# Performance work log

Hardware: AMD Instinct MI355X
Metric: run time of the kernel (lower is better)

Reference implementation:

```python
import jax, jax.numpy as jnp
import numpy as np

D_MODEL = 768
D_AU = 5
D_VIS = 20
BOT = 64
WIN = 7
SCALE = 1.0 / np.sqrt(BOT).astype(np.float32)


def layernorm(x, w, b, eps=1e-5):
    mu = jnp.mean(x, axis=-1, keepdims=True)
    var = jnp.mean(jnp.square(x - mu), axis=-1, keepdims=True)
    return (x - mu) * jax.lax.rsqrt(var + eps) * w + b


def proximity_bias_matrix(prox_bias, L_a, L_v):
    # |i * (L_v/L_a) - j|, floored to int; gather into learned table, -inf outside window
    ai = jnp.arange(L_a, dtype=jnp.float32) * (L_v / L_a)  # [L_a]
    vj = jnp.arange(L_v, dtype=jnp.float32)                # [L_v]
    dist = jnp.floor(jnp.abs(ai[:, None] - vj[None, :])).astype(jnp.int32)  # [L_a, L_v]
    within = dist <= WIN
    gathered = prox_bias[jnp.clip(dist, 0, 2 * WIN)]
    return jnp.where(within, gathered, -jnp.inf)


def setup_inputs() -> dict:
    key = jax.random.key(0)
    ks = jax.random.split(key, 32)
    B, L_t, L_v, L_a = 32, 1024, 1024, 2048
    std = 0.02
    inp = {
        'x_text': jax.random.normal(ks[0], (B, L_t, D_MODEL), jnp.float32),
        'video_features': jax.random.normal(ks[1], (B, L_v, D_VIS), jnp.float32),
        'audio_features': jax.random.normal(ks[2], (B, L_a, D_AU), jnp.float32),
        # adapter input LayerNorm (BERT init: weight=1, bias=0)
        'ln_w': jnp.ones((D_MODEL,), jnp.float32),
        'ln_b': jnp.zeros((D_MODEL,), jnp.float32),
        # down projections (torch Linear: [out, in])
        'dpa_w': std * jax.random.normal(ks[3], (BOT, D_AU), jnp.float32),
        'dpa_b': jnp.zeros((BOT,), jnp.float32),
        'dpv_w': std * jax.random.normal(ks[4], (BOT, D_VIS), jnp.float32),
        'dpv_b': jnp.zeros((BOT,), jnp.float32),
        # audio->video cross attention
        'wq_a': std * jax.random.normal(ks[5], (BOT, BOT), jnp.float32),
        'wk_v': std * jax.random.normal(ks[6], (BOT, BOT), jnp.float32),
        'wv_v': std * jax.random.normal(ks[7], (BOT, BOT), jnp.float32),
        'prox_bias': jnp.zeros((2 * WIN + 1,), jnp.float32),
        # fusion MLP + LN
        'fln_w': jnp.ones((2 * BOT,), jnp.float32),
        'fln_b': jnp.zeros((2 * BOT,), jnp.float32),
        'w1f_w': std * jax.random.normal(ks[8], (BOT, 2 * BOT), jnp.float32),
        'w1f_b': jnp.zeros((BOT,), jnp.float32),
        'w2f_w': std * jax.random.normal(ks[9], (BOT, BOT), jnp.float32),
        'w2f_b': jnp.zeros((BOT,), jnp.float32),
        # text->sync alignment attention
        'wq_t': std * jax.random.normal(ks[10], (BOT, D_MODEL), jnp.float32),
        'wk_s': std * jax.random.normal(ks[11], (BOT, BOT), jnp.float32),
        'wv_s': std * jax.random.normal(ks[12], (BOT, BOT), jnp.float32),
        # up projection + learnable scalar
        'up_w': std * jax.random.normal(ks[13], (D_MODEL, BOT), jnp.float32),
        'up_b': jnp.zeros((D_MODEL,), jnp.float32),
        'scale': jnp.ones((1,), jnp.float32),
    }
    return inp


def reference(x_text, video_features, audio_features, ln_w, ln_b, dpa_w, dpa_b,
              dpv_w, dpv_b, wq_a, wk_v, wv_v, prox_bias, fln_w, fln_b,
              w1f_w, w1f_b, w2f_w, w2f_b, wq_t, wk_s, wv_s, up_w, up_b, scale):
    L_v = video_features.shape[1]
    L_a = audio_features.shape[1]
    # adapter_layernorm_option == 'in'
    xt = layernorm(x_text, ln_w, ln_b)
    # down projections + ReLU
    H_v = jax.nn.relu(jnp.einsum('bvf,df->bvd', video_features, dpv_w) + dpv_b)
    H_a = jax.nn.relu(jnp.einsum('baf,df->bad', audio_features, dpa_w) + dpa_b)
    # audio queries attend to video keys/values with proximity bias
    Q_a = jnp.einsum('bad,ed->bae', H_a, wq_a)
    K_v = jnp.einsum('bvd,ed->bve', H_v, wk_v)
    V_v = jnp.einsum('bvd,ed->bve', H_v, wv_v)
    scores = jnp.einsum('bad,bvd->bav', Q_a, K_v) * SCALE
    scores = scores + proximity_bias_matrix(prox_bias, L_a, L_v)[None]
    A = jax.nn.softmax(scores, axis=-1)  # dropout: eval-mode identity
    H_v_tilde = jnp.einsum('bav,bvd->bad', A, V_v)
    # fusion
    H_av = jnp.concatenate([H_a, H_v_tilde], axis=-1)  # [B, L_a, 2*BOT]
    H_av_n = layernorm(H_av, fln_w, fln_b)
    H_fused = jax.nn.relu(jnp.einsum('bac,dc->bad', H_av_n, w1f_w) + w1f_b)
    H_sync = jnp.einsum('bad,ed->bae', H_fused, w2f_w) + w2f_b
    # text -> sync alignment attention
    Q_t = jnp.einsum('btm,dm->btd', xt, wq_t)
    K_s = jnp.einsum('bad,ed->bae', H_sync, wk_s)
    V_s = jnp.einsum('bad,ed->bae', H_sync, wv_s)
    align = jax.nn.softmax(jnp.einsum('btd,bad->bta', Q_t, K_s) * SCALE, axis=-1)
    H_align = jnp.einsum('bta,bad->btd', align, V_s)
    up = jnp.einsum('btd,md->btm', H_align, up_w) + up_b
    return up * scale
```

## Files before the change

kernel.cpp:

```cpp
#include <hip/hip_runtime.h>

typedef unsigned short u16;
typedef unsigned int u32;

using frag8 = __attribute__((ext_vector_type(8))) short;
using facc4 = __attribute__((ext_vector_type(4))) float;

__device__ __forceinline__ float b2f(u16 u) {
  union { u32 i; float f; } v; v.i = ((u32)u) << 16; return v.f;
}
__device__ __forceinline__ u16 f2b(float f) {
  union { float f; u32 i; } v; v.f = f;
  u32 u = v.i;
  return (u16)((u + 0x7FFFu + ((u >> 16) & 1u)) >> 16);
}
__device__ __forceinline__ float ldin(const void* p, size_t i, bool bf) {
  return bf ? b2f(((const u16*)p)[i]) : ((const float*)p)[i];
}
__device__ __forceinline__ u16 ldb(const void* p, size_t i, bool bf) {
  return bf ? ((const u16*)p)[i] : f2b(((const float*)p)[i]);
}
__device__ __forceinline__ bool dt_bf16(const void* ones) {
  return *(const u32*)ones == 0x3F803F80u;
}
__device__ __forceinline__ void gload_lds16(const void* g, void* l) {
  __builtin_amdgcn_global_load_lds(
      (__attribute__((address_space(1))) void*)(g),
      (__attribute__((address_space(3))) void*)(l), 16, 0, 0);
}

#define LT 1024
#define LV 1024
#define LA 2048
#define DM 768

#define W_QA 0
#define W_KV 4096
#define W_VV 8192
#define W_1F 12288
#define W_2F 20480
#define W_KS 24576
#define W_VS 28672
#define W_UP 32768
#define W_QT 81920
#define W_TOT 131072

__global__ __launch_bounds__(256) void k_prep(
    const void* __restrict__ wqa, const void* __restrict__ wkv, const void* __restrict__ wvv,
    const void* __restrict__ w1f, const void* __restrict__ w2f,
    const void* __restrict__ wks, const void* __restrict__ wvs,
    const void* __restrict__ wup, const void* __restrict__ wqt, const void* __restrict__ lnw,
    u16* __restrict__ W)
{
  bool bf = dt_bf16(lnw);
  int idx = blockIdx.x * 256 + threadIdx.x;
  if (idx >= W_TOT) return;
  u16 v;
  if      (idx < W_KV) v = ldb(wqa, idx - W_QA, bf);
  else if (idx < W_VV) v = ldb(wkv, idx - W_KV, bf);
  else if (idx < W_1F) v = ldb(wvv, idx - W_VV, bf);
  else if (idx < W_2F) v = ldb(w1f, idx - W_1F, bf);
  else if (idx < W_KS) v = ldb(w2f, idx - W_2F, bf);
  else if (idx < W_VS) v = ldb(wks, idx - W_KS, bf);
  else if (idx < W_UP) v = ldb(wvs, idx - W_VS, bf);
  else if (idx < W_QT) v = ldb(wup, idx - W_UP, bf);
  else {
    int r = idx - W_QT;
    int k = r - (r / DM) * DM;
    v = f2b(ldin(wqt, r, bf) * ldin(lnw, k, bf));
  }
  W[idx] = v;
}

__global__ __launch_bounds__(256) void k_const(
    const u16* __restrict__ W, const void* __restrict__ wqt, const void* __restrict__ lnb,
    const void* __restrict__ dtp, float* __restrict__ CC)
{
  bool bf = dt_bf16(dtp);
  int j = blockIdx.x * 8 + (threadIdx.x >> 5);
  int lane32 = threadIdx.x & 31;
  float s = 0.f;
  if (j < 64) {
    for (int k = lane32; k < DM; k += 32) s += b2f(W[W_QT + (size_t)j * DM + k]);
  } else {
    int e = j - 64;
    for (int k = lane32; k < DM; k += 32)
      s += ldin(lnb, k, bf) * ldin(wqt, (size_t)e * DM + k, bf);
  }
#pragma unroll
  for (int m = 1; m < 32; m <<= 1) s += __shfl_xor(s, m);
  if (lane32 == 0) CC[j] = s;
}

__global__ __launch_bounds__(256) void k_video(
    const void* __restrict__ vid, const void* __restrict__ dpv_w, const void* __restrict__ dpv_b,
    const u16* __restrict__ W, const void* __restrict__ dtp,
    u16* __restrict__ KvG, u16* __restrict__ VvTG)
{
  bool bf = dt_bf16(dtp);
  __shared__ float vidT[20][72];
  __shared__ float dpvT[20][72];
  __shared__ float dpvB[64];
  __shared__ u16 hvL[64][72];
  __shared__ u16 ksS[64][72];
  __shared__ u16 vsS[64][72];
  int tid = threadIdx.x;
  int b = blockIdx.x >> 4, v0 = (blockIdx.x & 15) << 6;
  for (int c = tid; c < 1280; c += 256) {
    int row = c / 20, d = c - row * 20;
    vidT[d][row] = ldin(vid, (size_t)(b * LV + v0) * 20 + c, bf);
    dpvT[d][row] = ldin(dpv_w, c, bf);
  }
  if (tid < 64) dpvB[tid] = ldin(dpv_b, tid, bf);
  __syncthreads();
  int w = tid >> 6, ln = tid & 63;
  int quad = ln >> 4, l16 = ln & 15;
  for (int rr = 0; rr < 16; ++rr) {
    int row = w * 16 + rr;
    float h = dpvB[ln];
#pragma unroll
    for (int d = 0; d < 20; ++d) h += vidT[d][row] * dpvT[d][ln];
    hvL[row][ln] = f2b(fmaxf(h, 0.f));
  }
  facc4 ka[4] = {}, va[4] = {};
#pragma unroll
  for (int kk = 0; kk < 2; ++kk) {
    frag8 af = *(const frag8*)&hvL[w * 16 + l16][kk * 32 + quad * 8];
#pragma unroll
    for (int nt = 0; nt < 4; ++nt) {
      frag8 bk = *(const frag8*)(W + W_KV + (size_t)(nt * 16 + l16) * 64 + kk * 32 + quad * 8);
      frag8 bv = *(const frag8*)(W + W_VV + (size_t)(nt * 16 + l16) * 64 + kk * 32 + quad * 8);
      ka[nt] = __builtin_amdgcn_mfma_f32_16x16x32_bf16(af, bk, ka[nt], 0, 0, 0);
      va[nt] = __builtin_amdgcn_mfma_f32_16x16x32_bf16(af, bv, va[nt], 0, 0, 0);
    }
  }
#pragma unroll
  for (int nt = 0; nt < 4; ++nt)
#pragma unroll
    for (int r = 0; r < 4; ++r) {
      int row = w * 16 + quad * 4 + r;
      ksS[row][nt * 16 + l16] = f2b(ka[nt][r]);
      vsS[row][nt * 16 + l16] = f2b(va[nt][r]);
    }
  __syncthreads();
  for (int c = tid; c < 2048; c += 256) {
    int row = c >> 5, sg = c & 31;
    u32 v = (u32)ksS[row][sg * 2] | ((u32)ksS[row][sg * 2 + 1] << 16);
    *(u32*)(KvG + (size_t)(b * LV + v0 + row) * 64 + sg * 2) = v;
  }
  for (int c = tid; c < 2048; c += 256) {
    int e = c >> 5, sg = c & 31;
    u32 v = (u32)vsS[sg * 2][e] | ((u32)vsS[sg * 2 + 1][e] << 16);
    *(u32*)(VvTG + (size_t)(b * 64 + e) * LV + v0 + sg * 2) = v;
  }
}

__global__ __launch_bounds__(256, 2) void k_lnqt(
    const void* __restrict__ x, const u16* __restrict__ W, const float* __restrict__ CC,
    const void* __restrict__ dtp, u16* __restrict__ Qt)
{
  bool bf = dt_bf16(dtp);
  int tid = threadIdx.x;
  int w = tid >> 6, ln = tid & 63;
  int quad = ln >> 4, l16 = ln & 15;
  int R0 = blockIdx.x * 64;
  const float* xrow = (const float*)x + (size_t)(R0 + w * 16 + l16) * DM + quad * 8;
  const u16* xrowb = (const u16*)x + (size_t)(R0 + w * 16 + l16) * DM + quad * 8;
  facc4 acc[4] = {};
  float s = 0.f, ss = 0.f;

  if (!bf) {
    float4 xa[16], xb[16];
#define LOADF(DST, G) \
    _Pragma("unroll") \
    for (int c = 0; c < 8; ++c) { \
      DST[2 * c]     = *(const float4*)(xrow + ((G) * 8 + c) * 32); \
      DST[2 * c + 1] = *(const float4*)(xrow + ((G) * 8 + c) * 32 + 4); \
    }
#define COMPF(SRC, G) \
    _Pragma("unroll") \
    for (int c = 0; c < 8; ++c) { \
      float4 v0 = SRC[2 * c], v1 = SRC[2 * c + 1]; \
      s += v0.x + v0.y + v0.z + v0.w + v1.x + v1.y + v1.z + v1.w; \
      ss += v0.x * v0.x + v0.y * v0.y + v0.z * v0.z + v0.w * v0.w \
          + v1.x * v1.x + v1.y * v1.y + v1.z * v1.z + v1.w * v1.w; \
      union { u16 a[8]; frag8 f; } af; \
      af.a[0] = f2b(v0.x); af.a[1] = f2b(v0.y); af.a[2] = f2b(v0.z); af.a[3] = f2b(v0.w); \
      af.a[4] = f2b(v1.x); af.a[5] = f2b(v1.y); af.a[6] = f2b(v1.z); af.a[7] = f2b(v1.w); \
      int col = ((G) * 8 + c) * 32 + quad * 8; \
      _Pragma("unroll") \
      for (int nt = 0; nt < 4; ++nt) { \
        frag8 bfr = *(const frag8*)(W + W_QT + (size_t)(nt * 16 + l16) * DM + col); \
        acc[nt] = __builtin_amdgcn_mfma_f32_16x16x32_bf16(af.f, bfr, acc[nt], 0, 0, 0); \
      } \
    }
    LOADF(xa, 0);
    LOADF(xb, 1);
    COMPF(xa, 0);
    LOADF(xa, 2);
    COMPF(xb, 1);
    COMPF(xa, 2);
#undef LOADF
#undef COMPF
  } else {
    frag8 xv[24];
#pragma unroll
    for (int c = 0; c < 24; ++c) xv[c] = *(const frag8*)(xrowb + c * 32);
#pragma unroll
    for (int c = 0; c < 24; ++c) {
      union { u16 a[8]; frag8 f; } af; af.f = xv[c];
#pragma unroll
      for (int jj = 0; jj < 8; ++jj) { float v = b2f(af.a[jj]); s += v; ss += v * v; }
      int col = c * 32 + quad * 8;
#pragma unroll
      for (int nt = 0; nt < 4; ++nt) {
        frag8 bfr = *(const frag8*)(W + W_QT + (size_t)(nt * 16 + l16) * DM + col);
        acc[nt] = __builtin_amdgcn_mfma_f32_16x16x32_bf16(xv[c], bfr, acc[nt], 0, 0, 0);
      }
    }
  }

  s += __shfl_xor(s, 16); ss += __shfl_xor(ss, 16);
  s += __shfl_xor(s, 32); ss += __shfl_xor(ss, 32);
  float mu = s * (1.f / 768.f);
  float var = ss * (1.f / 768.f) - mu * mu;
  float rs = rsqrtf(var + 1e-5f);
  float muR[4], rsR[4];
#pragma unroll
  for (int r = 0; r < 4; ++r) {
    muR[r] = __shfl(mu, quad * 4 + r);
    rsR[r] = __shfl(rs, quad * 4 + r);
  }
#pragma unroll
  for (int nt = 0; nt < 4; ++nt) {
    float c1 = CC[nt * 16 + l16], c2 = CC[64 + nt * 16 + l16];
#pragma unroll
    for (int r = 0; r < 4; ++r) {
      int lrow = w * 16 + quad * 4 + r;
      Qt[(size_t)(R0 + lrow) * 64 + nt * 16 + l16] =
          f2b((acc[nt][r] - muR[r] * c1) * rsR[r] * 0.125f + c2 * 0.125f);
    }
  }
}

__global__ __launch_bounds__(256) void k_audio(
    const void* __restrict__ audio, const void* __restrict__ dpa_w, const void* __restrict__ dpa_b,
    const void* __restrict__ prox_b,
    const void* __restrict__ fln_w, const void* __restrict__ fln_b,
    const void* __restrict__ w1f_b, const void* __restrict__ w2f_b,
    const u16* __restrict__ W, const void* __restrict__ dtp,
    const u16* __restrict__ KvG, const u16* __restrict__ VvTG,
    u16* __restrict__ KsG, u16* __restrict__ VsTG)
{
  bool bf = dt_bf16(dtp);
  __shared__ __align__(16) char pool[53056];
  u16* hL   = (u16*)pool;
  u16* kvB  = (u16*)(pool + 9216);
  u16* vvT  = (u16*)(pool + 16128);
  u16* qL   = (u16*)(pool + 25344);
  u16* hnL  = (u16*)(pool + 25344);
  u16* pfL  = (u16*)(pool + 42752);
  u16* hsS  = (u16*)(pool + 9216);
  u16* ksS  = (u16*)pool;
  u16* vsS  = (u16*)(pool + 9216);
  float* flnw = (float*)(pool + 51968);
  float* flnb = (float*)(pool + 52480);
  float* prox = (float*)(pool + 52992);

  int tid = threadIdx.x;
  int b = blockIdx.x >> 5, i0 = (blockIdx.x & 31) << 6;
  int w = tid >> 6, ln = tid & 63;
  int quad = ln >> 4, l16 = ln & 15;
  int jbase = (i0 >> 1) - 7;

  if (tid >= 64 && tid < 192) { int t = tid - 64; flnw[t] = ldin(fln_w, t, bf); flnb[t] = ldin(fln_b, t, bf); }
  if (tid >= 192 && tid < 207) prox[tid - 192] = ldin(prox_b, tid - 192, bf);
  for (int c = tid; c < 1536; c += 256) {
    int jr = c >> 5, ep = c & 31;
    int jj = jbase + jr; jj = jj < 0 ? 0 : (jj > LV - 1 ? LV - 1 : jj);
    *(u32*)&kvB[jr * 72 + ep * 2] = *(const u32*)(KvG + (size_t)(b * LV + jj) * 64 + ep * 2);
  }
  for (int c = tid; c < 3072; c += 256) {
    int e = c / 48, jw = c - e * 48;
    int jj = jbase + jw; jj = jj < 0 ? 0 : (jj > LV - 1 ? LV - 1 : jj);
    vvT[e * 72 + jw] = VvTG[(size_t)(b * 64 + e) * LV + jj];
  }
  for (int c = tid; c < 1024; c += 256) vvT[(c >> 4) * 72 + 48 + (c & 15)] = 0;
  __syncthreads();

  float haF[4][4];
  {
    frag8 au = {};
    if (quad == 0) {
      size_t base = (size_t)(b * LA + i0 + w * 16 + l16) * 5;
#pragma unroll
      for (int k = 0; k < 5; ++k) au[k] = (short)ldb(audio, base + k, bf);
    }
#pragma unroll
    for (int nt = 0; nt < 4; ++nt) {
      frag8 bd = {};
      if (quad == 0) {
#pragma unroll
        for (int k = 0; k < 5; ++k) bd[k] = (short)ldb(dpa_w, (size_t)(nt * 16 + l16) * 5 + k, bf);
      }
      facc4 z = {};
      facc4 ha = __builtin_amdgcn_mfma_f32_16x16x32_bf16(au, bd, z, 0, 0, 0);
      float dB = ldin(dpa_b, nt * 16 + l16, bf);
#pragma unroll
      for (int r = 0; r < 4; ++r) {
        u16 hb = f2b(fmaxf(ha[r] + dB, 0.f));
        hL[(w * 16 + quad * 4 + r) * 72 + nt * 16 + l16] = hb;
        haF[nt][r] = b2f(hb);
      }
    }
  }
  {
    facc4 qa[4] = {};
#pragma unroll
    for (int kk = 0; kk < 2; ++kk) {
      frag8 af = *(const frag8*)&hL[(w * 16 + l16) * 72 + kk * 32 + quad * 8];
#pragma unroll
      for (int nt = 0; nt < 4; ++nt) {
        frag8 bfr = *(const frag8*)(W + W_QA + (size_t)(nt * 16 + l16) * 64 + kk * 32 + quad * 8);
        qa[nt] = __builtin_amdgcn_mfma_f32_16x16x32_bf16(af, bfr, qa[nt], 0, 0, 0);
      }
    }
#pragma unroll
    for (int nt = 0; nt < 4; ++nt)
#pragma unroll
      for (int r = 0; r < 4; ++r)
        qL[(w * 16 + quad * 4 + r) * 72 + nt * 16 + l16] = f2b(qa[nt][r] * 0.125f);
  }
  float inv[4];
  {
    facc4 sa[3] = {};
#pragma unroll
    for (int kk = 0; kk < 2; ++kk) {
      frag8 af = *(const frag8*)&qL[(w * 16 + l16) * 72 + kk * 32 + quad * 8];
#pragma unroll
      for (int nt = 0; nt < 3; ++nt) {
        frag8 bfr = *(const frag8*)&kvB[(nt * 16 + l16) * 72 + kk * 32 + quad * 8];
        sa[nt] = __builtin_amdgcn_mfma_f32_16x16x32_bf16(af, bfr, sa[nt], 0, 0, 0);
      }
    }
    float den[4] = {0.f, 0.f, 0.f, 0.f};
#pragma unroll
    for (int nt = 0; nt < 3; ++nt)
#pragma unroll
      for (int r = 0; r < 4; ++r) {
        int row16 = quad * 4 + r;
        int i = i0 + w * 16 + row16;
        int j = jbase + nt * 16 + l16;
        float dist = fabsf((float)i * 0.5f - (float)j);
        float p = 0.f;
        if (j >= 0 && j < LV && dist < 8.f)
          p = exp2f(fminf(sa[nt][r] + prox[(int)dist], 60.f) * 1.44269504f);
        u16 pb = f2b(p);
        den[r] += b2f(pb);
        pfL[(w * 16 + row16) * 72 + nt * 16 + l16] = pb;
      }
#pragma unroll
    for (int r = 0; r < 4; ++r) {
      pfL[(w * 16 + quad * 4 + r) * 72 + 48 + l16] = 0;
#pragma unroll
      for (int m = 1; m < 16; m <<= 1) den[r] += __shfl_xor(den[r], m);
      inv[r] = 1.f / den[r];
    }
  }
  float hvF[4][4];
  {
    facc4 ha[4] = {};
#pragma unroll
    for (int kk = 0; kk < 2; ++kk) {
      frag8 af = *(const frag8*)&pfL[(w * 16 + l16) * 72 + kk * 32 + quad * 8];
#pragma unroll
      for (int nt = 0; nt < 4; ++nt) {
        frag8 bfr = *(const frag8*)&vvT[(nt * 16 + l16) * 72 + kk * 32 + quad * 8];
        ha[nt] = __builtin_amdgcn_mfma_f32_16x16x32_bf16(af, bfr, ha[nt], 0, 0, 0);
      }
    }
#pragma unroll
    for (int nt = 0; nt < 4; ++nt)
#pragma unroll
      for (int r = 0; r < 4; ++r) {
        u16 hb = f2b(ha[nt][r] * inv[r]);
        hvF[nt][r] = b2f(hb);
      }
  }
  __syncthreads();
#pragma unroll
  for (int r = 0; r < 4; ++r) {
    float s = 0.f, ss = 0.f;
#pragma unroll
    for (int nt = 0; nt < 4; ++nt) {
      float a = haF[nt][r], c = hvF[nt][r];
      s += a + c; ss += a * a + c * c;
    }
#pragma unroll
    for (int m = 1; m < 16; m <<= 1) { s += __shfl_xor(s, m); ss += __shfl_xor(ss, m); }
    float mu = s * (1.f / 128.f);
    float var = ss * (1.f / 128.f) - mu * mu;
    float rs = rsqrtf(var + 1e-5f);
    int row = w * 16 + quad * 4 + r;
#pragma unroll
    for (int nt = 0; nt < 4; ++nt) {
      int col = nt * 16 + l16;
      hnL[row * 136 + col]      = f2b((haF[nt][r] - mu) * rs * flnw[col] + flnb[col]);
      hnL[row * 136 + 64 + col] = f2b((hvF[nt][r] - mu) * rs * flnw[64 + col] + flnb[64 + col]);
    }
  }
  {
    facc4 f1[4] = {};
#pragma unroll
    for (int kk = 0; kk < 4; ++kk) {
      frag8 af = *(const frag8*)&hnL[(w * 16 + l16) * 136 + kk * 32 + quad * 8];
#pragma unroll
      for (int nt = 0; nt < 4; ++nt) {
        frag8 bfr = *(const frag8*)(W + W_1F + (size_t)(nt * 16 + l16) * 128 + kk * 32 + quad * 8);
        f1[nt] = __builtin_amdgcn_mfma_f32_16x16x32_bf16(af, bfr, f1[nt], 0, 0, 0);
      }
    }
#pragma unroll
    for (int nt = 0; nt < 4; ++nt) {
      float b1 = ldin(w1f_b, nt * 16 + l16, bf);
#pragma unroll
      for (int r = 0; r < 4; ++r)
        pfL[(w * 16 + quad * 4 + r) * 72 + nt * 16 + l16] = f2b(fmaxf(f1[nt][r] + b1, 0.f));
    }
  }
  {
    facc4 f2[4] = {};
#pragma unroll
    for (int kk = 0; kk < 2; ++kk) {
      frag8 af = *(const frag8*)&pfL[(w * 16 + l16) * 72 + kk * 32 + quad * 8];
#pragma unroll
      for (int nt = 0; nt < 4; ++nt) {
        frag8 bfr = *(const frag8*)(W + W_2F + (size_t)(nt * 16 + l16) * 64 + kk * 32 + quad * 8);
        f2[nt] = __builtin_amdgcn_mfma_f32_16x16x32_bf16(af, bfr, f2[nt], 0, 0, 0);
      }
    }
#pragma unroll
    for (int nt = 0; nt < 4; ++nt) {
      float b2 = ldin(w2f_b, nt * 16 + l16, bf);
#pragma unroll
      for (int r = 0; r < 4; ++r)
        hsS[(w * 16 + quad * 4 + r) * 72 + nt * 16 + l16] = f2b(f2[nt][r] + b2);
    }
  }
  {
    facc4 fk[4] = {}, fv[4] = {};
#pragma unroll
    for (int kk = 0; kk < 2; ++kk) {
      frag8 af = *(const frag8*)&hsS[(w * 16 + l16) * 72 + kk * 32 + quad * 8];
#pragma unroll
      for (int nt = 0; nt < 4; ++nt) {
        frag8 bk = *(const frag8*)(W + W_KS + (size_t)(nt * 16 + l16) * 64 + kk * 32 + quad * 8);
        frag8 bv = *(const frag8*)(W + W_VS + (size_t)(nt * 16 + l16) * 64 + kk * 32 + quad * 8);
        fk[nt] = __builtin_amdgcn_mfma_f32_16x16x32_bf16(af, bk, fk[nt], 0, 0, 0);
        fv[nt] = __builtin_amdgcn_mfma_f32_16x16x32_bf16(af, bv, fv[nt], 0, 0, 0);
      }
    }
#pragma unroll
    for (int nt = 0; nt < 4; ++nt)
#pragma unroll
      for (int r = 0; r < 4; ++r) {
        int row = w * 16 + quad * 4 + r;
        ksS[row * 72 + nt * 16 + l16] = f2b(fk[nt][r]);
        vsS[row * 72 + nt * 16 + l16] = f2b(fv[nt][r]);
      }
  }
  __syncthreads();
  for (int c = tid; c < 2048; c += 256) {
    int row = c >> 5, sg = c & 31;
    u32 v = (u32)ksS[row * 72 + sg * 2] | ((u32)ksS[row * 72 + sg * 2 + 1] << 16);
    *(u32*)(KsG + (size_t)(b * LA + i0 + row) * 64 + sg * 2) = v;
  }
  for (int c = tid; c < 2048; c += 256) {
    int e = c >> 5, sg = c & 31;
    u32 v = (u32)vsS[sg * 2 * 72 + e] | ((u32)vsS[(sg * 2 + 1) * 72 + e] << 16);
    *(u32*)(VsTG + (size_t)(b * 64 + e) * LA + i0 + sg * 2) = v;
  }
}

#define KS_OFF 0
#define VT_OFF 16384
#define PO_OFF 32768

__global__ __launch_bounds__(256, 4) void k_attn_p(
    const u16* __restrict__ Qt, const u16* __restrict__ KsG, const u16* __restrict__ VsT,
    u16* __restrict__ OpG, float* __restrict__ DenG)
{
  __shared__ __align__(16) char pool[40960];
  int tid = threadIdx.x, w = tid >> 6, ln = tid & 63;
  int quad = ln >> 4, l16 = ln & 15;
  int pb = blockIdx.x;
  int b = pb >> 5, tt = (pb >> 1) & 15, half = pb & 1;
  int t0 = tt << 6;
  const u16* qp = Qt + (size_t)(b * LT + t0 + w * 16 + l16) * 64;
  frag8 qf0 = *(const frag8*)(qp + quad * 8);
  frag8 qf1 = *(const frag8*)(qp + 32 + quad * 8);

  int r8 = ln >> 3;
  int sgx = (ln & 7) ^ r8;
  const char* kg0 = (const char*)KsG +
      (((size_t)(b * LA + half * 1024 + w * 16 + r8)) << 7) + sgx * 16;
  const char* kg1 = kg0 + 1024;
  const char* vg0 = (const char*)VsT +
      (((size_t)(b * 64 + w * 16 + r8)) * LA + half * 1024 + sgx * 8) * 2;
  const char* vg1 = vg0 + (size_t)8 * LA * 2;

#define STAGE(BUF, TT) do { \
    size_t ko_ = (size_t)(TT) * 8192, vo_ = (size_t)(TT) * 128; \
    gload_lds16(kg0 + ko_, pool + KS_OFF + (BUF) * 8192 + w * 2048); \
    gload_lds16(kg1 + ko_, pool + KS_OFF + (BUF) * 8192 + w * 2048 + 1024); \
    gload_lds16(vg0 + vo_, pool + VT_OFF + (BUF) * 8192 + w * 2048); \
    gload_lds16(vg1 + vo_, pool + VT_OFF + (BUF) * 8192 + w * 2048 + 1024); \
  } while (0)

  int l8 = l16 & 7, lh = l16 >> 3;
  int swl = l8 << 4;
  int koff0 = l16 * 128 + ((quad * 16) ^ swl);
  int koff1 = l16 * 128 + ((64 + quad * 16) ^ swl);
  int pro0 = w * 2048 + l16 * 128 + ((quad ^ l8) << 4);
  int pro1 = w * 2048 + l16 * 128 + (((4 + quad) ^ l8) << 4);
  int pwb = w * 2048 + quad * 512 + l8 * 2;

  facc4 oacc[4] = {};
  float den[4] = {0.f, 0.f, 0.f, 0.f};

#define COMPUTE(CUR) do { \
    const char* ksp_ = pool + KS_OFF + (CUR) * 8192; \
    const char* vtp_ = pool + VT_OFF + (CUR) * 8192; \
    __builtin_amdgcn_s_setprio(1); \
    _Pragma("unroll") \
    for (int nt = 0; nt < 4; ++nt) { \
      frag8 b0 = *(const frag8*)(ksp_ + koff0 + nt * 2048); \
      frag8 b1 = *(const frag8*)(ksp_ + koff1 + nt * 2048); \
      facc4 sv = {}; \
      sv = __builtin_amdgcn_mfma_f32_16x16x32_bf16(qf0, b0, sv, 0, 0, 0); \
      sv = __builtin_amdgcn_mfma_f32_16x16x32_bf16(qf1, b1, sv, 0, 0, 0); \
      _Pragma("unroll") \
      for (int r = 0; r < 4; ++r) { \
        float p = exp2f(fminf(sv[r], 60.f) * 1.44269504f); \
        u16 pb_ = f2b(p); \
        den[r] += b2f(pb_); \
        int rm_ = ((quad & 1) << 2) + r; \
        *(u16*)(pool + PO_OFF + pwb + r * 128 + (((nt * 2 + lh) ^ rm_) << 4)) = pb_; \
      } \
    } \
    _Pragma("unroll") \
    for (int kk = 0; kk < 2; ++kk) { \
      frag8 af = *(const frag8*)(pool + PO_OFF + (kk ? pro1 : pro0)); \
      _Pragma("unroll") \
      for (int nt = 0; nt < 4; ++nt) { \
        frag8 bv = *(const frag8*)(vtp_ + (kk ? koff1 : koff0) + nt * 2048); \
        oacc[nt] = __builtin_amdgcn_mfma_f32_16x16x32_bf16(af, bv, oacc[nt], 0, 0, 0); \
      } \
    } \
    __builtin_amdgcn_s_setprio(0); \
  } while (0)

#define ITERS(TT, CUR) do { \
    asm volatile("s_waitcnt vmcnt(0)" ::: "memory"); \
    __builtin_amdgcn_s_barrier(); \
    STAGE((CUR) ^ 1, (TT) + 1); \
    COMPUTE(CUR); \
  } while (0)

  STAGE(0, 0);
  for (int t2 = 0; t2 < 14; t2 += 2) {
    ITERS(t2, 0);
    ITERS(t2 + 1, 1);
  }
  ITERS(14, 0);
  asm volatile("s_waitcnt vmcnt(0)" ::: "memory");
  __builtin_amdgcn_s_barrier();
  COMPUTE(1);

#undef ITERS
#undef COMPUTE
#undef STAGE

#pragma unroll
  for (int m = 1; m < 16; m <<= 1)
#pragma unroll
    for (int r = 0; r < 4; ++r) den[r] += __shfl_xor(den[r], m);
  if (l16 == 0) {
#pragma unroll
    for (int r = 0; r < 4; ++r)
      DenG[(size_t)pb * 64 + w * 16 + quad * 4 + r] = den[r];
  }
#pragma unroll
  for (int nt = 0; nt < 4; ++nt)
#pragma unroll
    for (int r = 0; r < 4; ++r)
      OpG[(size_t)pb * 4096 + (w * 16 + quad * 4 + r) * 64 + nt * 16 + l16] =
          f2b(oacc[nt][r]);
}

__global__ __launch_bounds__(256) void k_up(
    const u16* __restrict__ OpG, const float* __restrict__ DenG,
    const u16* __restrict__ W, const void* __restrict__ up_b,
    const void* __restrict__ scaleP, const void* __restrict__ dtp, void* __restrict__ outp)
{
  bool bf = dt_bf16(dtp);
  int tid = threadIdx.x, w = tid >> 6, ln = tid & 63;
  int quad = ln >> 4, l16 = ln & 15;
  int g = blockIdx.x;
  int b = g >> 5, tt = (g >> 1) & 15, nh = g & 1;
  int t0 = tt << 6;
  int blk = b * 16 + tt;
  int row = w * 16 + l16;
  const u16* p0 = OpG + ((size_t)blk * 2 + 0) * 4096 + row * 64;
  const u16* p1 = p0 + 4096;
  float dsum = DenG[(size_t)blk * 128 + row] + DenG[(size_t)blk * 128 + 64 + row];
  float inv = 1.f / dsum;
  union { u16 a[8]; frag8 f; } a0, a1;
  {
    frag8 u0 = *(const frag8*)(p0 + quad * 8);
    frag8 u1 = *(const frag8*)(p1 + quad * 8);
    frag8 v0 = *(const frag8*)(p0 + 32 + quad * 8);
    frag8 v1 = *(const frag8*)(p1 + 32 + quad * 8);
#pragma unroll
    for (int j = 0; j < 8; ++j) {
      a0.a[j] = f2b((b2f((u16)u0[j]) + b2f((u16)u1[j])) * inv);
      a1.a[j] = f2b((b2f((u16)v0[j]) + b2f((u16)v1[j])) * inv);
    }
  }
  float scl = ldin(scaleP, 0, bf);
  u16* o16 = (u16*)outp;
  float* o32 = (float*)outp;
  for (int nt = nh * 24; nt < nh * 24 + 24; ++nt) {
    frag8 b0f = *(const frag8*)(W + W_UP + (size_t)(nt * 16 + l16) * 64 + quad * 8);
    frag8 b1f = *(const frag8*)(W + W_UP + (size_t)(nt * 16 + l16) * 64 + 32 + quad * 8);
    facc4 d = {};
    d = __builtin_amdgcn_mfma_f32_16x16x32_bf16(a0.f, b0f, d, 0, 0, 0);
    d = __builtin_amdgcn_mfma_f32_16x16x32_bf16(a1.f, b1f, d, 0, 0, 0);
    float ub = ldin(up_b, nt * 16 + l16, bf);
#pragma unroll
    for (int r = 0; r < 4; ++r) {
      int t = t0 + w * 16 + quad * 4 + r;
      size_t idx = ((size_t)(b * LT) + t) * DM + nt * 16 + l16;
      float v = (d[r] + ub) * scl;
      if (bf) o16[idx] = f2b(v); else o32[idx] = v;
    }
  }
}

extern "C" void kernel_launch(void* const* d_in, const int* in_sizes, int n_in,
                              void* d_out, int out_size, void* d_ws, size_t ws_size,
                              hipStream_t stream) {
  const void* x_text = d_in[0];
  const void* video  = d_in[1];
  const void* audio  = d_in[2];
  const void* ln_w   = d_in[3];
  const void* ln_b   = d_in[4];
  const void* dpa_w  = d_in[5];
  const void* dpa_b  = d_in[6];
  const void* dpv_w  = d_in[7];
  const void* dpv_b  = d_in[8];
  const void* wq_a   = d_in[9];
  const void* wk_v   = d_in[10];
  const void* wv_v   = d_in[11];
  const void* prox   = d_in[12];
  const void* fln_w  = d_in[13];
  const void* fln_b  = d_in[14];
  const void* w1f_w  = d_in[15];
  const void* w1f_b  = d_in[16];
  const void* w2f_w  = d_in[17];
  const void* w2f_b  = d_in[18];
  const void* wq_t   = d_in[19];
  const void* wk_s   = d_in[20];
  const void* wv_s   = d_in[21];
  const void* up_w   = d_in[22];
  const void* up_b   = d_in[23];
  const void* scale  = d_in[24];

  char* ws = (char*)d_ws;
  u16* KvG  = (u16*)(ws);
  u16* VvTG = (u16*)(ws + 4194304);
  u16* Qt   = (u16*)(ws + 8388608);
  u16* KsG  = (u16*)(ws + 12582912);
  u16* VsTG = (u16*)(ws + 20971520);
  u16* W    = (u16*)(ws + 29360128);
  float* CC = (float*)(ws + 29622272);
  u16* OpG  = (u16*)(ws);
  float* DenG = (float*)(ws + 29622784);

  k_prep <<<dim3(512), dim3(256), 0, stream>>>(wq_a, wk_v, wv_v, w1f_w, w2f_w,
                                               wk_s, wv_s, up_w, wq_t, ln_w, W);
  k_const<<<dim3(16),  dim3(256), 0, stream>>>(W, wq_t, ln_b, ln_w, CC);
  k_video<<<dim3(512), dim3(256), 0, stream>>>(video, dpv_w, dpv_b, W, ln_w, KvG, VvTG);
  k_lnqt <<<dim3(512), dim3(256), 0, stream>>>(x_text, W, CC, ln_w, Qt);
  k_audio<<<dim3(1024), dim3(256), 0, stream>>>(audio, dpa_w, dpa_b, prox,
                                                fln_w, fln_b, w1f_b, w2f_b,
                                                W, ln_w, KvG, VvTG, KsG, VsTG);
  k_attn_p<<<dim3(1024), dim3(256), 0, stream>>>(Qt, KsG, VsTG, OpG, DenG);
  k_up   <<<dim3(1024), dim3(256), 0, stream>>>(OpG, DenG, W, up_b, scale, ln_w, d_out);
}
```

Before: 400.0 us.

## Stage text rows through LDS with triple-buffered async global loads in LN+Q kernel

The fp32 path of the text LayerNorm + Q projection kernel now streams x through a 48KB shared-memory pool. It uses direct global-to-LDS loads, three buffers and an XOR-swizzled layout, and waits on vmcnt with barriers between stages. This replaces the large register-held float4 prefetch arrays, which aims to cut register pressure and overlap HBM reads with MFMA work. The cost is extra LDS usage that may limit occupancy, plus barrier overhead. The bf16 path drops its 24-register preload.

```diff
diff --git a/kernel.cpp b/kernel.cpp
--- a/kernel.cpp
+++ b/kernel.cpp
@@ -160,62 +160,96 @@
     const void* __restrict__ dtp, u16* __restrict__ Qt)
 {
   bool bf = dt_bf16(dtp);
+  __shared__ __align__(16) char pool[49152];
   int tid = threadIdx.x;
   int w = tid >> 6, ln = tid & 63;
   int quad = ln >> 4, l16 = ln & 15;
   int R0 = blockIdx.x * 64;
-  const float* xrow = (const float*)x + (size_t)(R0 + w * 16 + l16) * DM + quad * 8;
-  const u16* xrowb = (const u16*)x + (size_t)(R0 + w * 16 + l16) * DM + quad * 8;
   facc4 acc[4] = {};
   float s = 0.f, ss = 0.f;
 
   if (!bf) {
-    float4 xa[16], xb[16];
-#define LOADF(DST, G) \
+    int rqe = ln >> 4;
+    const char* xb = (const char*)x + (size_t)R0 * 3072;
+    const char* pe = xb + (size_t)(w * 16 + rqe) * 3072 + (((ln & 15) ^ rqe) << 4);
+    const char* po = xb + (size_t)(w * 16 + 4 + rqe) * 3072 + (((ln & 15) ^ (4 + rqe)) << 4);
+
+#define STAGE(BUF, T) do { \
+    size_t o_ = (size_t)(T) * 256; \
+    char* lb_ = pool + (BUF) * 16384 + w * 4096; \
+    gload_lds16(pe + o_,         lb_); \
+    gload_lds16(po + o_,         lb_ + 1024); \
+    gload_lds16(pe + 24576 + o_, lb_ + 2048); \
+    gload_lds16(po + 24576 + o_, lb_ + 3072); \
+  } while (0)
+
+    int rw = w * 16 + l16;
+    int rbase = rw * 256;
+    int r8 = l16 & 7;
+    int c0a = rbase + (((quad * 2) ^ r8) << 4);
+    int c0b = rbase + (((quad * 2 + 1) ^ r8) << 4);
+    int c1a = rbase + (((8 + quad * 2) ^ r8) << 4);
+    int c1b = rbase + (((9 + quad * 2) ^ r8) << 4);
+    const char* wq = (const char*)(W + W_QT + (size_t)l16 * DM + quad * 8);
+
+#define COMPUTE(CUR) do { \
+    const char* xt_ = pool + (CUR) * 16384; \
     _Pragma("unroll") \
-    for (int c = 0; c < 8; ++c) { \
-      DST[2 * c]     = *(const float4*)(xrow + ((G) * 8 + c) * 32); \
-      DST[2 * c + 1] = *(const float4*)(xrow + ((G) * 8 + c) * 32 + 4); \
-    }
-#define COMPF(SRC, G) \
-    _Pragma("unroll") \
-    for (int c = 0; c < 8; ++c) { \
-      float4 v0 = SRC[2 * c], v1 = SRC[2 * c + 1]; \
+    for (int ks = 0; ks < 2; ++ks) { \
+      float4 v0 = *(const float4*)(xt_ + (ks ? c1a : c0a)); \
+      float4 v1 = *(const float4*)(xt_ + (ks ? c1b : c0b)); \
       s += v0.x + v0.y + v0.z + v0.w + v1.x + v1.y + v1.z + v1.w; \
       ss += v0.x * v0.x + v0.y * v0.y + v0.z * v0.z + v0.w * v0.w \
           + v1.x * v1.x + v1.y * v1.y + v1.z * v1.z + v1.w * v1.w; \
       union { u16 a[8]; frag8 f; } af; \
       af.a[0] = f2b(v0.x); af.a[1] = f2b(v0.y); af.a[2] = f2b(v0.z); af.a[3] = f2b(v0.w); \
       af.a[4] = f2b(v1.x); af.a[5] = f2b(v1.y); af.a[6] = f2b(v1.z); af.a[7] = f2b(v1.w); \
-      int col = ((G) * 8 + c) * 32 + quad * 8; \
       _Pragma("unroll") \
       for (int nt = 0; nt < 4; ++nt) { \
-        frag8 bfr = *(const frag8*)(W + W_QT + (size_t)(nt * 16 + l16) * DM + col); \
+        frag8 bfr = *(const frag8*)(wq + nt * 24576 + ks * 64); \
         acc[nt] = __builtin_amdgcn_mfma_f32_16x16x32_bf16(af.f, bfr, acc[nt], 0, 0, 0); \
       } \
-    }
-    LOADF(xa, 0);
-    LOADF(xb, 1);
-    COMPF(xa, 0);
-    LOADF(xa, 2);
-    COMPF(xb, 1);
-    COMPF(xa, 2);
-#undef LOADF
-#undef COMPF
+    } \
+    wq += 128; \
+  } while (0)
+
+#define ITERX(T, CUR, NXT) do { \
+    asm volatile("s_waitcnt vmcnt(4)" ::: "memory"); \
+    __builtin_amdgcn_s_barrier(); \
+    STAGE(NXT, (T) + 2); \
+    COMPUTE(CUR); \
+  } while (0)
+
+    STAGE(0, 0);
+    STAGE(1, 1);
+    for (int t3 = 0; t3 < 9; t3 += 3) {
+      ITERX(t3 + 0, 0, 2);
+      ITERX(t3 + 1, 1, 0);
+      ITERX(t3 + 2, 2, 1);
+    }
+    ITERX(9, 0, 2);
+    asm volatile("s_waitcnt vmcnt(4)" ::: "memory");
+    __builtin_amdgcn_s_barrier();
+    COMPUTE(1);
+    asm volatile("s_waitcnt vmcnt(0)" ::: "memory");
+    __builtin_amdgcn_s_barrier();
+    COMPUTE(2);
+
+#undef ITERX
+#undef COMPUTE
+#undef STAGE
   } else {
-    frag8 xv[24];
-#pragma unroll
-    for (int c = 0; c < 24; ++c) xv[c] = *(const frag8*)(xrowb + c * 32);
-#pragma unroll
+    const u16* xrowb = (const u16*)x + (size_t)(R0 + w * 16 + l16) * DM + quad * 8;
     for (int c = 0; c < 24; ++c) {
-      union { u16 a[8]; frag8 f; } af; af.f = xv[c];
+      union { u16 a[8]; frag8 f; } af;
+      af.f = *(const frag8*)(xrowb + c * 32);
 #pragma unroll
       for (int jj = 0; jj < 8; ++jj) { float v = b2f(af.a[jj]); s += v; ss += v * v; }
       int col = c * 32 + quad * 8;
 #pragma unroll
       for (int nt = 0; nt < 4; ++nt) {
         frag8 bfr = *(const frag8*)(W + W_QT + (size_t)(nt * 16 + l16) * DM + col);
-        acc[nt] = __builtin_amdgcn_mfma_f32_16x16x32_bf16(xv[c], bfr, acc[nt], 0, 0, 0);
+        acc[nt] = __builtin_amdgcn_mfma_f32_16x16x32_bf16(af.f, bfr, acc[nt], 0, 0, 0);
       }
     }
   }
```

Measured after the change: 396.6 us. No clear change (-0.8%).
